# Kernel optimization log

Measured on AMD Instinct MI355X. Metric: run time of the kernel, lower is better.

## Reference

```python
import jax, jax.numpy as jnp
import numpy as np

NUM_GRAPHS = 512

def gcn_conv(x, src, dst, W, b, n):
    # x: [N, Fin], W: [Fin, Fout]. PyG GCNConv: add self loops, symmetric norm.
    h = x @ W  # [N, Fout]
    loop = jnp.arange(n)
    s = jnp.concatenate([src, loop])
    d = jnp.concatenate([dst, loop])
    ones = jnp.ones(s.shape[0], dtype=h.dtype)
    deg = jax.ops.segment_sum(ones, d, num_segments=n)  # includes self loop -> >= 1
    dinv = jax.lax.rsqrt(deg)
    norm = dinv[s] * dinv[d]  # [E+N]
    msg = h[s] * norm[:, None]  # gather + scale (memory-bound)
    out = jax.ops.segment_sum(msg, d, num_segments=n)
    return out + b

def setup_inputs() -> dict:
    key = jax.random.key(0)
    ks = jax.random.split(key, 10)
    N, E, F, H, O, EF = 100000, 1600000, 128, 128, 1, 16
    x = jax.random.normal(ks[0], (N, F), dtype=jnp.float32)
    edge_index = jax.random.randint(ks[1], (2, E), 0, N)
    edge_attr = jax.random.normal(ks[2], (E, EF), dtype=jnp.float32)
    batch = jnp.sort(jax.random.randint(ks[3], (N,), 0, NUM_GRAPHS))
    s1 = 1.0 / np.sqrt(F)
    s2 = 1.0 / np.sqrt(H)
    W1 = jax.random.uniform(ks[4], (F, H), jnp.float32, -s1, s1)
    b1 = jnp.zeros((H,), jnp.float32)
    W2 = jax.random.uniform(ks[5], (H, H), jnp.float32, -s2, s2)
    b2 = jnp.zeros((H,), jnp.float32)
    Wl = jax.random.uniform(ks[6], (H, O), jnp.float32, -s2, s2)
    bl = jnp.zeros((O,), jnp.float32)
    return {"x": x, "edge_index": edge_index, "edge_attr": edge_attr, "batch": batch,
            "W1": W1, "b1": b1, "W2": W2, "b2": b2, "Wl": Wl, "bl": bl}

def reference(x, edge_index, edge_attr, batch, W1, b1, W2, b2, Wl, bl):
    n = x.shape[0]
    src, dst = edge_index[0], edge_index[1]
    h = jax.nn.relu(gcn_conv(x, src, dst, W1, b1, n))
    h = gcn_conv(h, src, dst, W2, b2, n)
    # global mean pool by graph id
    summed = jax.ops.segment_sum(h, batch, num_segments=NUM_GRAPHS)  # [G, H]
    counts = jax.ops.segment_sum(jnp.ones((n,), h.dtype), batch, num_segments=NUM_GRAPHS)
    pooled = summed / jnp.maximum(counts, 1.0)[:, None]
    return pooled @ Wl + bl  # [G, 1]
```

## Files before the change

kernel.cpp:

```cpp
#include <hip/hip_runtime.h>


typedef __attribute__((ext_vector_type(8))) short short8;
typedef __attribute__((ext_vector_type(4))) float f32x4;

#define CHUNK 4096
#define RW    128

__device__ __forceinline__ unsigned short bf16r(float f) {
    unsigned u = __float_as_uint(f);
    u += 0x7FFFu + ((u >> 16) & 1u);
    return (unsigned short)(u >> 16);
}

__device__ __forceinline__ float bff(unsigned short u) {
    return __uint_as_float((unsigned)u << 16);
}

__global__ void k_w2l(const float* __restrict__ W2, const float* __restrict__ Wl,
                      float* __restrict__ w2l) {
    int i = threadIdx.x;
    float s = 0.0f;
    for (int j = 0; j < 128; ++j) s = fmaf(W2[i * 128 + j], Wl[j], s);
    w2l[i] = s;
}

__global__ void k_w1pack(const float* __restrict__ W1, unsigned short* __restrict__ w1p) {
    int idx = blockIdx.x * blockDim.x + threadIdx.x;
    if (idx < 16384) {
        int k = idx >> 7, n = idx & 127;
        w1p[((k >> 3) * 128 + n) * 8 + (k & 7)] = bf16r(W1[idx]);
    }
}

__global__ __launch_bounds__(256) void k_part(
    const int* __restrict__ src, const int* __restrict__ dst,
    int2* __restrict__ part, int* __restrict__ off_t, int* __restrict__ cnt_t,
    int E, int nchunks, int NR)
{
    __shared__ int2 stage[CHUNK];
    __shared__ int lcnt[1024];
    __shared__ int lscan[1024];
    int tid = threadIdx.x;
    int j = blockIdx.x;
    int base = j * CHUNK;

#pragma unroll
    for (int k = 0; k < 4; ++k) lcnt[tid + k * 256] = 0;
    __syncthreads();

    int mys[16], myd[16], myr[16];
#pragma unroll
    for (int k = 0; k < 16; ++k) {
        int e = base + tid + (k << 8);
        bool ok = e < E;
        int s = ok ? src[e] : 0;
        int d = ok ? dst[e] : 0;
        int r = -1;
        if (ok) {
            r = d >> 7;
            atomicAdd(&lcnt[r], 1);
        }
        mys[k] = s; myd[k] = d; myr[k] = r;
    }
    __syncthreads();

    int* pa = lcnt;
    int* pb = lscan;
    for (int off = 1; off < 1024; off <<= 1) {
#pragma unroll
        for (int k = 0; k < 4; ++k) {
            int idx = tid + k * 256;
            int v = pa[idx];
            if (idx >= off) v += pa[idx - off];
            pb[idx] = v;
        }
        __syncthreads();
        int* tmp = pa; pa = pb; pb = tmp;
    }
    for (int i = tid; i < NR; i += 256) {
        int incl = pa[i];
        int excl = (i == 0) ? 0 : pa[i - 1];
        pb[i] = excl;
        off_t[(size_t)i * nchunks + j] = excl;
        cnt_t[(size_t)i * nchunks + j] = incl - excl;
    }
    __syncthreads();

#pragma unroll
    for (int k = 0; k < 16; ++k) {
        if (myr[k] >= 0) {
            int p = atomicAdd(&pb[myr[k]], 1);
            stage[p] = make_int2(mys[k], myd[k]);
        }
    }
    __syncthreads();

    int valid = E - base; if (valid > CHUNK) valid = CHUNK;
    for (int i = tid; i < valid; i += 256)
        part[(size_t)base + i] = stage[i];
}

__global__ __launch_bounds__(64) void k_rtot(
    const int* __restrict__ cnt_t, int* __restrict__ rtot, int nchunks)
{
    int r = blockIdx.x;
    int lane = threadIdx.x;
    const int* row = cnt_t + (size_t)r * nchunks;
    int s = 0;
    for (int j = lane; j < nchunks; j += 64) s += row[j];
#pragma unroll
    for (int off = 32; off > 0; off >>= 1) s += __shfl_xor(s, off);
    if (lane == 0) rtot[r] = s;
}

__global__ __launch_bounds__(1024) void k_rbase(
    const int* __restrict__ rtot, int* __restrict__ rbase, int NR)
{
    __shared__ int a1[1024], a2[1024];
    int tid = threadIdx.x;
    a1[tid] = (tid < NR) ? rtot[tid] : 0;
    __syncthreads();
    int* pa = a1; int* pb = a2;
    for (int off = 1; off < 1024; off <<= 1) {
        int v = pa[tid];
        if (tid >= off) v += pa[tid - off];
        pb[tid] = v;
        __syncthreads();
        int* tmp = pa; pa = pb; pb = tmp;
    }
    if (tid < NR) rbase[tid] = (tid == 0) ? 0 : pa[tid - 1];
    if (tid == 0) rbase[NR] = pa[NR >= 1 ? NR - 1 : 0];
}

__global__ __launch_bounds__(256) void k_rscat(
    const int2* __restrict__ part, const int* __restrict__ off_t,
    const int* __restrict__ cnt_t, const int* __restrict__ rbase,
    int* __restrict__ srt, int* __restrict__ rp, float* __restrict__ dinv,
    int nchunks, int N, int NR, int E)
{
    __shared__ int hist[RW], lcur[RW], s1[RW], s2[RW];
    int r = blockIdx.x;
    int tid = threadIdx.x;
    int d0 = r << 7;
    int width = N - d0; if (width > RW) width = RW;
    if (tid < RW) hist[tid] = 0;
    __syncthreads();

    const int* orow = off_t + (size_t)r * nchunks;
    const int* crow = cnt_t + (size_t)r * nchunks;

    for (int j = tid; j < nchunks; j += 256) {
        int o0 = orow[j], c = crow[j];
        const int2* pp = part + (size_t)j * CHUNK + o0;
        for (int e = 0; e < c; ++e)
            atomicAdd(&hist[pp[e].y - d0], 1);
    }
    __syncthreads();

    if (tid < RW) s1[tid] = hist[tid];
    __syncthreads();
    int* pa = s1; int* pb = s2;
    for (int off = 1; off < RW; off <<= 1) {
        if (tid < RW) {
            int v = pa[tid];
            if (tid >= off) v += pa[tid - off];
            pb[tid] = v;
        }
        __syncthreads();
        int* tmp = pa; pa = pb; pb = tmp;
    }
    if (tid < width) {
        int excl = (tid == 0) ? 0 : pa[tid - 1];
        int start = rbase[r] + excl;
        rp[d0 + tid] = start;
        lcur[tid] = start;
        dinv[d0 + tid] = 1.0f / sqrtf((float)hist[tid] + 1.0f);
    }
    if (r == 0 && tid == 0) rp[N] = E;
    __syncthreads();

    for (int j = tid; j < nchunks; j += 256) {
        int o0 = orow[j], c = crow[j];
        const int2* pp = part + (size_t)j * CHUNK + o0;
        for (int e = 0; e < c; ++e) {
            int2 ed = pp[e];
            int pos = atomicAdd(&lcur[ed.y - d0], 1);
            srt[pos] = ed.x;
        }
    }
}

__global__ __launch_bounds__(256) void k_mm_mfma(
    const float* __restrict__ A, const unsigned short* __restrict__ w1p,
    const float* __restrict__ dinv, unsigned short* __restrict__ C, int N)
{
    __shared__ unsigned short w1s[16384];
    int tid = threadIdx.x;
    {
        const uint4* s = (const uint4*)w1p;
        uint4* d = (uint4*)w1s;
#pragma unroll
        for (int i = 0; i < 8; ++i) d[tid + i * 256] = s[tid + i * 256];
    }
    __syncthreads();

    int w = tid >> 6, lane = tid & 63;
    int m = lane & 15, quad = lane >> 4;
    int r0 = blockIdx.x * 128 + w * 32;

    f32x4 acc[2][8];
#pragma unroll
    for (int rg = 0; rg < 2; ++rg)
#pragma unroll
        for (int cg = 0; cg < 8; ++cg) {
            f32x4 z = {0.0f, 0.0f, 0.0f, 0.0f};
            acc[rg][cg] = z;
        }

#pragma unroll
    for (int ks = 0; ks < 4; ++ks) {
        int k0 = ks * 32 + quad * 8;
        short8 a[2];
#pragma unroll
        for (int rg = 0; rg < 2; ++rg) {
            int r = r0 + rg * 16 + m;
            if (r > N - 1) r = N - 1;
            const float* ap = A + (size_t)r * 128 + k0;
            float4 v0 = *(const float4*)ap;
            float4 v1 = *(const float4*)(ap + 4);
            short8 av;
            av[0] = (short)bf16r(v0.x); av[1] = (short)bf16r(v0.y);
            av[2] = (short)bf16r(v0.z); av[3] = (short)bf16r(v0.w);
            av[4] = (short)bf16r(v1.x); av[5] = (short)bf16r(v1.y);
            av[6] = (short)bf16r(v1.z); av[7] = (short)bf16r(v1.w);
            a[rg] = av;
        }
        int kc = ks * 4 + quad;
#pragma unroll
        for (int cg = 0; cg < 8; ++cg) {
            const short8* bp = (const short8*)&w1s[((size_t)kc * 128 + cg * 16 + m) * 8];
            short8 b = *bp;
            acc[0][cg] = __builtin_amdgcn_mfma_f32_16x16x32_bf16(a[0], b, acc[0][cg], 0, 0, 0);
            acc[1][cg] = __builtin_amdgcn_mfma_f32_16x16x32_bf16(a[1], b, acc[1][cg], 0, 0, 0);
        }
    }

#pragma unroll
    for (int rg = 0; rg < 2; ++rg) {
        int rbase2 = r0 + rg * 16 + quad * 4;
#pragma unroll
        for (int reg = 0; reg < 4; ++reg) {
            int r = rbase2 + reg;
            if (r < N) {
                float s = dinv[r];
#pragma unroll
                for (int cg = 0; cg < 8; ++cg)
                    C[(size_t)r * 128 + cg * 16 + m] = bf16r(acc[rg][cg][reg] * s);
            }
        }
    }
}

__global__ __launch_bounds__(256) void k_agg1(
    const unsigned short* __restrict__ t, const float* __restrict__ dinv,
    const int* __restrict__ rp, const int* __restrict__ srt,
    const float* __restrict__ b1, const float* __restrict__ w2l,
    float* __restrict__ q, int N)
{
    __shared__ int shi[4][64];
    int wave = threadIdx.x >> 6;
    int lane = threadIdx.x & 63;
    int node = blockIdx.x * 4 + wave;
    if (node >= N) return;
    int s0 = rp[node], s1 = rp[node + 1];
    int deg = s1 - s0;
    int vdeg = deg < 63 ? deg : 63;

    int idx = N;
    if (lane < vdeg) idx = srt[s0 + lane];
    else if (lane == vdeg) idx = node;
    shi[wave][lane] = idx;
    const int* shw = shi[wave];

    int r4 = lane >> 4;
    int c = lane & 15;
    const unsigned short* tc = t + c * 8;

    float a[8];
#pragma unroll
    for (int k = 0; k < 8; ++k) a[k] = 0.0f;

    int nrows = vdeg + 1;
    int nquads = (nrows + 3) >> 2;
    int p = 0;

    while (p + 8 <= nquads) {
        short8 v[8];
#pragma unroll
        for (int j = 0; j < 8; ++j) {
            int id = shw[((p + j) << 2) + r4];
            v[j] = *(const short8*)(tc + (size_t)id * 128);
        }
#pragma unroll
        for (int j = 0; j < 8; ++j)
#pragma unroll
            for (int k = 0; k < 8; ++k)
                a[k] += bff((unsigned short)v[j][k]);
        p += 8;
    }
    if (p + 4 <= nquads) {
        short8 v[4];
#pragma unroll
        for (int j = 0; j < 4; ++j) {
            int id = shw[((p + j) << 2) + r4];
            v[j] = *(const short8*)(tc + (size_t)id * 128);
        }
#pragma unroll
        for (int j = 0; j < 4; ++j)
#pragma unroll
            for (int k = 0; k < 8; ++k)
                a[k] += bff((unsigned short)v[j][k]);
        p += 4;
    }
    if (p + 2 <= nquads) {
        short8 v[2];
#pragma unroll
        for (int j = 0; j < 2; ++j) {
            int id = shw[((p + j) << 2) + r4];
            v[j] = *(const short8*)(tc + (size_t)id * 128);
        }
#pragma unroll
        for (int j = 0; j < 2; ++j)
#pragma unroll
            for (int k = 0; k < 8; ++k)
                a[k] += bff((unsigned short)v[j][k]);
        p += 2;
    }
    if (p < nquads) {
        int id = shw[(p << 2) + r4];
        short8 v = *(const short8*)(tc + (size_t)id * 128);
#pragma unroll
        for (int k = 0; k < 8; ++k)
            a[k] += bff((unsigned short)v[k]);
    }
    if (deg > 63) {
        for (int e = s0 + 63; e < s1; ++e) {
            int id = srt[e];
            short8 v = *(const short8*)(tc + (size_t)id * 128);
            if (r4 == 0)
#pragma unroll
                for (int k = 0; k < 8; ++k)
                    a[k] += bff((unsigned short)v[k]);
        }
    }

#pragma unroll
    for (int k = 0; k < 8; ++k) {
        a[k] += __shfl_xor(a[k], 16);
        a[k] += __shfl_xor(a[k], 32);
    }

    float di = dinv[node];
    float4 b0 = *(const float4*)(b1 + c * 8);
    float4 b4 = *(const float4*)(b1 + c * 8 + 4);
    float4 w0 = *(const float4*)(w2l + c * 8);
    float4 w4 = *(const float4*)(w2l + c * 8 + 4);
    float pr = 0.0f;
    pr += fmaxf(fmaf(a[0], di, b0.x), 0.0f) * w0.x;
    pr += fmaxf(fmaf(a[1], di, b0.y), 0.0f) * w0.y;
    pr += fmaxf(fmaf(a[2], di, b0.z), 0.0f) * w0.z;
    pr += fmaxf(fmaf(a[3], di, b0.w), 0.0f) * w0.w;
    pr += fmaxf(fmaf(a[4], di, b4.x), 0.0f) * w4.x;
    pr += fmaxf(fmaf(a[5], di, b4.y), 0.0f) * w4.y;
    pr += fmaxf(fmaf(a[6], di, b4.z), 0.0f) * w4.z;
    pr += fmaxf(fmaf(a[7], di, b4.w), 0.0f) * w4.w;
#pragma unroll
    for (int off = 8; off > 0; off >>= 1) pr += __shfl_xor(pr, off);
    if (lane == 0) q[node] = pr * di;
}

__global__ __launch_bounds__(256) void k_agg2(
    const float* __restrict__ q, const float* __restrict__ dinv,
    const int* __restrict__ rp, const int* __restrict__ srt,
    float* __restrict__ p, int N)
{
    int tid = blockIdx.x * 256 + threadIdx.x;
    int node = tid >> 4;
    int l = tid & 15;
    if (node >= N) return;
    int s0 = rp[node], s1 = rp[node + 1];
    float a = 0.0f;
    for (int e = s0 + l; e < s1; e += 16) a += q[srt[e]];
#pragma unroll
    for (int off = 8; off > 0; off >>= 1) a += __shfl_xor(a, off);
    if (l == 0) p[node] = dinv[node] * (a + q[node]);
}

__global__ __launch_bounds__(64) void k_pool(
    const float* __restrict__ p, const int* __restrict__ batch,
    const float* __restrict__ b2, const float* __restrict__ Wl,
    const float* __restrict__ bl, float* __restrict__ out, int N, int G)
{
    int g = blockIdx.x;
    int lane = threadIdx.x;
    __shared__ int sb[2];
    if (lane < 2) {
        int target = g + lane;
        int lo = 0, hi = N;
        while (lo < hi) {
            int mid = (lo + hi) >> 1;
            if (batch[mid] < target) lo = mid + 1; else hi = mid;
        }
        sb[lane] = lo;
    }
    __syncthreads();
    int s = sb[0], e = sb[1];
    float a = 0.0f;
    for (int i = s + lane; i < e; i += 64) a += p[i];
#pragma unroll
    for (int off = 32; off > 0; off >>= 1) a += __shfl_xor(a, off);
    if (lane == 0) {
        float c = 0.0f;
        for (int j = 0; j < 128; ++j) c = fmaf(b2[j], Wl[j], c);
        out[g] = a / fmaxf((float)(e - s), 1.0f) + c + bl[0];
    }
}

extern "C" void kernel_launch(void* const* d_in, const int* in_sizes, int n_in,
                              void* d_out, int out_size, void* d_ws, size_t ws_size,
                              hipStream_t stream)
{
    const float* x  = (const float*)d_in[0];
    const int*   ei = (const int*)d_in[1];
    const int*   batch = (const int*)d_in[3];
    const float* W1 = (const float*)d_in[4];
    const float* b1 = (const float*)d_in[5];
    const float* W2 = (const float*)d_in[6];
    const float* b2 = (const float*)d_in[7];
    const float* Wl = (const float*)d_in[8];
    const float* bl = (const float*)d_in[9];

    int N = in_sizes[0] / 128;
    int E = in_sizes[1] / 2;
    const int* src = ei;
    const int* dst = ei + E;

    char* ws = (char*)d_ws;
    size_t off = 0;
    auto alloc = [&](size_t bytes) -> void* {
        void* p = ws + off;
        off = (off + bytes + 255) & ~(size_t)255;
        return p;
    };
    int nchunks = (E + CHUNK - 1) / CHUNK;
    int NR = (N + RW - 1) / RW;
    unsigned short* t = (unsigned short*)alloc((size_t)(N + 1) * 128 * 2);
    float* q    = (float*)alloc((size_t)N * 4);
    float* p    = (float*)alloc((size_t)N * 4);
    int*   srt  = (int*)alloc((size_t)E * 4);
    int2*  part = (int2*)alloc((size_t)nchunks * CHUNK * 8);
    int*   off_t= (int*)alloc((size_t)NR * nchunks * 4);
    int*   cnt_t= (int*)alloc((size_t)NR * nchunks * 4);
    int*   rtot = (int*)alloc((size_t)NR * 4);
    int*   rbase= (int*)alloc((size_t)(NR + 1) * 4);
    float* dinv = (float*)alloc((size_t)N * 4);
    int*   rp   = (int*)alloc((size_t)(N + 1) * 4);
    float* w2l  = (float*)alloc(128 * 4);
    unsigned short* w1p = (unsigned short*)alloc(16384 * 2);
    (void)ws_size;

    hipMemsetAsync(t + (size_t)N * 128, 0, 256, stream);

    k_part<<<nchunks, 256, 0, stream>>>(src, dst, part, off_t, cnt_t, E, nchunks, NR);
    k_w2l<<<1, 128, 0, stream>>>(W2, Wl, w2l);
    k_w1pack<<<64, 256, 0, stream>>>(W1, w1p);
    k_rtot<<<NR, 64, 0, stream>>>(cnt_t, rtot, nchunks);
    k_rbase<<<1, 1024, 0, stream>>>(rtot, rbase, NR);
    k_rscat<<<NR, 256, 0, stream>>>(part, off_t, cnt_t, rbase, srt, rp, dinv,
                                    nchunks, N, NR, E);

    int mmb = (N + 127) / 128;
    k_mm_mfma<<<mmb, 256, 0, stream>>>(x, w1p, dinv, t, N);
    k_agg1<<<(N + 3) / 4, 256, 0, stream>>>(t, dinv, rp, srt, b1, w2l, q, N);
    k_agg2<<<((size_t)N * 16 + 255) / 256, 256, 0, stream>>>(q, dinv, rp, srt, p, N);
    k_pool<<<512, 64, 0, stream>>>(p, batch, b2, Wl, bl, (float*)d_out, N, 512);
}
```

Measured before the change: 344.3 us.

## Pack edges into one int, stage bucket edges in LDS, merge weight-prep kernels

Edges are packed as (src<<7)|(dst&127), which halves the partition buffer traffic. The row-scatter kernel now stages its bucket's edges in shared memory during the histogram pass, so the scatter pass reads them from LDS instead of re-reading global memory, with a global fallback on overflow. The W2·Wl and W1-pack kernels are merged into a single launch. The aggregation tail branches are replaced by an 8-wide do-while, which relies on padded index slots and may issue extra loads for low-degree nodes. Packing assumes src < 2^24.

```diff
diff --git a/kernel.cpp b/kernel.cpp
--- a/kernel.cpp
+++ b/kernel.cpp
@@ -6,6 +6,8 @@
 
 #define CHUNK 4096
 #define RW    128
+#define SCAP  6144
+#define JCAP  512
 
 __device__ __forceinline__ unsigned short bf16r(float f) {
     unsigned u = __float_as_uint(f);
@@ -17,28 +19,29 @@
     return __uint_as_float((unsigned)u << 16);
 }
 
-__global__ void k_w2l(const float* __restrict__ W2, const float* __restrict__ Wl,
-                      float* __restrict__ w2l) {
-    int i = threadIdx.x;
-    float s = 0.0f;
-    for (int j = 0; j < 128; ++j) s = fmaf(W2[i * 128 + j], Wl[j], s);
-    w2l[i] = s;
-}
-
-__global__ void k_w1pack(const float* __restrict__ W1, unsigned short* __restrict__ w1p) {
-    int idx = blockIdx.x * blockDim.x + threadIdx.x;
-    if (idx < 16384) {
-        int k = idx >> 7, n = idx & 127;
-        w1p[((k >> 3) * 128 + n) * 8 + (k & 7)] = bf16r(W1[idx]);
-    }
+__global__ void k_w1pack(const float* __restrict__ W1, unsigned short* __restrict__ w1p,
+                         const float* __restrict__ W2, const float* __restrict__ Wl,
+                         float* __restrict__ w2l) {
+    if (blockIdx.x == 64) {
+        int i = threadIdx.x;
+        if (i < 128) {
+            float s = 0.0f;
+            for (int j = 0; j < 128; ++j) s = fmaf(W2[i * 128 + j], Wl[j], s);
+            w2l[i] = s;
+        }
+        return;
+    }
+    int idx = blockIdx.x * 256 + threadIdx.x;
+    int k = idx >> 7, n = idx & 127;
+    w1p[((k >> 3) * 128 + n) * 8 + (k & 7)] = bf16r(W1[idx]);
 }
 
 __global__ __launch_bounds__(256) void k_part(
     const int* __restrict__ src, const int* __restrict__ dst,
-    int2* __restrict__ part, int* __restrict__ off_t, int* __restrict__ cnt_t,
+    int* __restrict__ part, int* __restrict__ off_t, int* __restrict__ cnt_t,
     int E, int nchunks, int NR)
 {
-    __shared__ int2 stage[CHUNK];
+    __shared__ int stage[CHUNK];
     __shared__ int lcnt[1024];
     __shared__ int lscan[1024];
     int tid = threadIdx.x;
@@ -49,7 +52,7 @@
     for (int k = 0; k < 4; ++k) lcnt[tid + k * 256] = 0;
     __syncthreads();
 
-    int mys[16], myd[16], myr[16];
+    int mye[16], myr[16];
 #pragma unroll
     for (int k = 0; k < 16; ++k) {
         int e = base + tid + (k << 8);
@@ -61,7 +64,8 @@
             r = d >> 7;
             atomicAdd(&lcnt[r], 1);
         }
-        mys[k] = s; myd[k] = d; myr[k] = r;
+        mye[k] = (s << 7) | (d & 127);
+        myr[k] = r;
     }
     __syncthreads();
 
@@ -91,7 +95,7 @@
     for (int k = 0; k < 16; ++k) {
         if (myr[k] >= 0) {
             int p = atomicAdd(&pb[myr[k]], 1);
-            stage[p] = make_int2(mys[k], myd[k]);
+            stage[p] = mye[k];
         }
     }
     __syncthreads();
@@ -134,29 +138,41 @@
 }
 
 __global__ __launch_bounds__(256) void k_rscat(
-    const int2* __restrict__ part, const int* __restrict__ off_t,
+    const int* __restrict__ part, const int* __restrict__ off_t,
     const int* __restrict__ cnt_t, const int* __restrict__ rbase,
     int* __restrict__ srt, int* __restrict__ rp, float* __restrict__ dinv,
-    int nchunks, int N, int NR, int E)
-{
+    int nchunks, int N, int E)
+{
+    __shared__ int stage[SCAP];
+    __shared__ int jbase[JCAP];
     __shared__ int hist[RW], lcur[RW], s1[RW], s2[RW];
+    __shared__ int cursor;
     int r = blockIdx.x;
     int tid = threadIdx.x;
     int d0 = r << 7;
     int width = N - d0; if (width > RW) width = RW;
     if (tid < RW) hist[tid] = 0;
+    if (tid == 0) cursor = 0;
     __syncthreads();
 
     const int* orow = off_t + (size_t)r * nchunks;
     const int* crow = cnt_t + (size_t)r * nchunks;
 
     for (int j = tid; j < nchunks; j += 256) {
-        int o0 = orow[j], c = crow[j];
-        const int2* pp = part + (size_t)j * CHUNK + o0;
-        for (int e = 0; e < c; ++e)
-            atomicAdd(&hist[pp[e].y - d0], 1);
-    }
-    __syncthreads();
+        int c = crow[j];
+        if (c == 0) { if (j < JCAP) jbase[j] = 0; continue; }
+        int b = (j < JCAP) ? atomicAdd(&cursor, c) : SCAP;
+        if (j < JCAP) jbase[j] = b;
+        const int* pp = part + (size_t)j * CHUNK + orow[j];
+        for (int e = 0; e < c; ++e) {
+            int ed = pp[e];
+            int pos = b + e;
+            if (pos < SCAP) stage[pos] = ed;
+            atomicAdd(&hist[ed & 127], 1);
+        }
+    }
+    __syncthreads();
+    int total = cursor;
 
     if (tid < RW) s1[tid] = hist[tid];
     __syncthreads();
@@ -180,13 +196,29 @@
     if (r == 0 && tid == 0) rp[N] = E;
     __syncthreads();
 
-    for (int j = tid; j < nchunks; j += 256) {
-        int o0 = orow[j], c = crow[j];
-        const int2* pp = part + (size_t)j * CHUNK + o0;
-        for (int e = 0; e < c; ++e) {
-            int2 ed = pp[e];
-            int pos = atomicAdd(&lcur[ed.y - d0], 1);
-            srt[pos] = ed.x;
+    int lim = total < SCAP ? total : SCAP;
+    for (int i = tid; i < lim; i += 256) {
+        int ed = stage[i];
+        int pos = atomicAdd(&lcur[ed & 127], 1);
+        srt[pos] = ed >> 7;
+    }
+    if (total > SCAP || nchunks > JCAP) {
+        for (int j = tid; j < nchunks; j += 256) {
+            int c = crow[j];
+            if (c == 0) continue;
+            int e0 = 0;
+            if (j < JCAP) {
+                int b = jbase[j];
+                e0 = SCAP - b;
+                if (e0 < 0) e0 = 0;
+                if (e0 >= c) continue;
+            }
+            const int* pp = part + (size_t)j * CHUNK + orow[j];
+            for (int e = e0; e < c; ++e) {
+                int ed = pp[e];
+                int pos = atomicAdd(&lcur[ed & 127], 1);
+                srt[pos] = ed >> 7;
+            }
         }
     }
 }
@@ -294,8 +326,7 @@
     int nrows = vdeg + 1;
     int nquads = (nrows + 3) >> 2;
     int p = 0;
-
-    while (p + 8 <= nquads) {
+    do {
         short8 v[8];
 #pragma unroll
         for (int j = 0; j < 8; ++j) {
@@ -308,42 +339,8 @@
             for (int k = 0; k < 8; ++k)
                 a[k] += bff((unsigned short)v[j][k]);
         p += 8;
-    }
-    if (p + 4 <= nquads) {
-        short8 v[4];
-#pragma unroll
-        for (int j = 0; j < 4; ++j) {
-            int id = shw[((p + j) << 2) + r4];
-            v[j] = *(const short8*)(tc + (size_t)id * 128);
-        }
-#pragma unroll
-        for (int j = 0; j < 4; ++j)
-#pragma unroll
-            for (int k = 0; k < 8; ++k)
-                a[k] += bff((unsigned short)v[j][k]);
-        p += 4;
-    }
-    if (p + 2 <= nquads) {
-        short8 v[2];
-#pragma unroll
-        for (int j = 0; j < 2; ++j) {
-            int id = shw[((p + j) << 2) + r4];
-            v[j] = *(const short8*)(tc + (size_t)id * 128);
-        }
-#pragma unroll
-        for (int j = 0; j < 2; ++j)
-#pragma unroll
-            for (int k = 0; k < 8; ++k)
-                a[k] += bff((unsigned short)v[j][k]);
-        p += 2;
-    }
-    if (p < nquads) {
-        int id = shw[(p << 2) + r4];
-        short8 v = *(const short8*)(tc + (size_t)id * 128);
-#pragma unroll
-        for (int k = 0; k < 8; ++k)
-            a[k] += bff((unsigned short)v[k]);
-    }
+    } while (p < nquads);
+
     if (deg > 63) {
         for (int e = s0 + 63; e < s1; ++e) {
             int id = srt[e];
@@ -459,7 +456,7 @@
     float* q    = (float*)alloc((size_t)N * 4);
     float* p    = (float*)alloc((size_t)N * 4);
     int*   srt  = (int*)alloc((size_t)E * 4);
-    int2*  part = (int2*)alloc((size_t)nchunks * CHUNK * 8);
+    int*   part = (int*)alloc((size_t)nchunks * CHUNK * 4);
     int*   off_t= (int*)alloc((size_t)NR * nchunks * 4);
     int*   cnt_t= (int*)alloc((size_t)NR * nchunks * 4);
     int*   rtot = (int*)alloc((size_t)NR * 4);
@@ -473,12 +470,11 @@
     hipMemsetAsync(t + (size_t)N * 128, 0, 256, stream);
 
     k_part<<<nchunks, 256, 0, stream>>>(src, dst, part, off_t, cnt_t, E, nchunks, NR);
-    k_w2l<<<1, 128, 0, stream>>>(W2, Wl, w2l);
-    k_w1pack<<<64, 256, 0, stream>>>(W1, w1p);
+    k_w1pack<<<65, 256, 0, stream>>>(W1, w1p, W2, Wl, w2l);
     k_rtot<<<NR, 64, 0, stream>>>(cnt_t, rtot, nchunks);
     k_rbase<<<1, 1024, 0, stream>>>(rtot, rbase, NR);
     k_rscat<<<NR, 256, 0, stream>>>(part, off_t, cnt_t, rbase, srt, rp, dinv,
-                                    nchunks, N, NR, E);
+                                    nchunks, N, E);
 
     int mmb = (N + 127) / 128;
     k_mm_mfma<<<mmb, 256, 0, stream>>>(x, w1p, dinv, t, N);
```

Measured after the change: 337.9 us. About the same (-1.9%).
